# Optimization experiments

Measured on AMD Instinct MI355X. Metric: run time of the kernel, lower is better.

Reference implementation:

```python
import jax, jax.numpy as jnp
import numpy as np

N = 10000        # nodes
E = 320000       # edges (avg degree 32)
NF_IN = 256
NF_OUT = 512
EPS = 1e-5


def batch_norm(x, gamma, beta):
    # BatchNorm1d training-mode: biased stats over the node (batch) dim
    mu = jnp.mean(x, axis=0)
    var = jnp.var(x, axis=0)
    return (x - mu) * jax.lax.rsqrt(var + EPS) * gamma + beta


def sage_conv(x, src, dst, W_l, W_r, bias):
    # PyG SAGEConv, aggr='mean': out = lin_l(mean_{j->i} x_j) + lin_r(x_i)
    msg = x[src]                                             # [E, F]
    s = jax.ops.segment_sum(msg, dst, num_segments=N)        # [N, F]
    cnt = jax.ops.segment_sum(jnp.ones((msg.shape[0], 1), x.dtype), dst, num_segments=N)
    mean = s / jnp.maximum(cnt, 1.0)
    return mean @ W_l + bias + x @ W_r


def setup_inputs() -> dict:
    key = jax.random.key(0)
    ks = jax.random.split(key, 8)
    x = jax.random.normal(ks[0], (N, NF_IN), jnp.float32)
    edge_index = jax.random.randint(ks[1], (2, E), 0, N, dtype=jnp.int64)
    s_in = 0.02
    return {
        "x": x,
        "edge_index": edge_index,
        "gamma0": jnp.ones((NF_IN,), jnp.float32),
        "beta0": jnp.zeros((NF_IN,), jnp.float32),
        "W0_l": jax.random.normal(ks[2], (NF_IN, NF_OUT), jnp.float32) * s_in,
        "W0_r": jax.random.normal(ks[3], (NF_IN, NF_OUT), jnp.float32) * s_in,
        "bias0": jnp.zeros((NF_OUT,), jnp.float32),
        "gamma1": jnp.ones((NF_OUT,), jnp.float32),
        "beta1": jnp.zeros((NF_OUT,), jnp.float32),
        "W1_l": jax.random.normal(ks[4], (NF_OUT, NF_OUT), jnp.float32) * s_in,
        "W1_r": jax.random.normal(ks[5], (NF_OUT, NF_OUT), jnp.float32) * s_in,
        "bias1": jnp.zeros((NF_OUT,), jnp.float32),
        "W_sc": jax.random.normal(ks[6], (NF_IN, NF_OUT), jnp.float32) * s_in,
        "b_sc": jnp.zeros((NF_OUT,), jnp.float32),
    }


def reference(x, edge_index, gamma0, beta0, W0_l, W0_r, bias0,
              gamma1, beta1, W1_l, W1_r, bias1, W_sc, b_sc):
    src, dst = edge_index[0], edge_index[1]
    h = jax.nn.relu(batch_norm(x, gamma0, beta0))
    h = sage_conv(h, src, dst, W0_l, W0_r, bias0)
    h = jax.nn.relu(batch_norm(h, gamma1, beta1))
    h = sage_conv(h, src, dst, W1_l, W1_r, bias1)
    x_sc = x @ W_sc + b_sc  # nin_shortcut since nf_in != nf_out
    return x_sc + h
```

## Files before the change

kernel.cpp:

```cpp
#include <hip/hip_runtime.h>
#include <hip/hip_bf16.h>
#include <cstdint>
#include <cstddef>

#define N_NODES 10000
#define N_EDGES 320000
#define FIN 256
#define FOUT 512
#define BN_EPS 1e-5f
#define DEG_CAP 96
#define SLICE_CAP 18
#define NRANGES 20
#define NSLICES 16
#define NODES_PER_RANGE (N_NODES / NRANGES)
#define EDGES_PER_SLICE (N_EDGES / NSLICES)
#define SCAN_BLOCKS (NRANGES * NSLICES)

typedef unsigned short ushort_t;
typedef unsigned char uchar_t;
typedef __attribute__((ext_vector_type(8))) short short8;
typedef __attribute__((ext_vector_type(16))) float f32x16;
typedef __attribute__((ext_vector_type(2))) float f32x2;
typedef __attribute__((ext_vector_type(4))) unsigned short ushort4v;
typedef __attribute__((ext_vector_type(8))) unsigned short ushort8v;

__device__ inline ushort_t f2bf(float f) {
  __hip_bfloat16 h = __float2bfloat16(f);
  return *reinterpret_cast<ushort_t*>(&h);
}
__device__ inline float bf2f(ushort_t u) {
  union { unsigned int i; float f; } c;
  c.i = ((unsigned int)u) << 16;
  return c.f;
}
__device__ inline uchar_t f2q(float v) {
  return (uchar_t)(__builtin_amdgcn_cvt_pk_fp8_f32(v, v, 0u, false) & 0xffu);
}
__device__ inline void q4_to_f32(unsigned int w, float* o) {
  f32x2 lo = __builtin_amdgcn_cvt_pk_f32_fp8(w, false);
  f32x2 hi = __builtin_amdgcn_cvt_pk_f32_fp8(w, true);
  o[0] = lo[0]; o[1] = lo[1]; o[2] = hi[0]; o[3] = hi[1];
}

__global__ void zero_k(int* __restrict__ p, int n) {
  int i = blockIdx.x * blockDim.x + threadIdx.x;
  if (i < n) p[i] = 0;
}

__global__ __launch_bounds__(256)
void prologue_k(const int* __restrict__ src, const int* __restrict__ dst,
                int* __restrict__ fill, int* __restrict__ csrc,
                const float* __restrict__ W0l, const float* __restrict__ W0r,
                const float* __restrict__ Wsc, const float* __restrict__ W1l,
                const float* __restrict__ W1r, const float* __restrict__ bias1,
                const float* __restrict__ bsc,
                ushort_t* __restrict__ w0lt, ushort_t* __restrict__ w0rt,
                ushort_t* __restrict__ wsct, ushort_t* __restrict__ w1lt,
                ushort_t* __restrict__ w1rt, float* __restrict__ cbias,
                const float* __restrict__ x, float* __restrict__ sums0,
                ushort_t* __restrict__ xb, uchar_t* __restrict__ xq) {
  __shared__ __align__(16) char smem[512 * 4 + NODES_PER_RANGE * SLICE_CAP * 4];
  int b = blockIdx.x;
  int tid = threadIdx.x;

  if (b < SCAN_BLOCKS) {
    int range = b / NSLICES;
    int slice = b % NSLICES;
    int lo = range * NODES_PER_RANGE;
    int* lcnt = (int*)smem;
    int* lbuf = lcnt + 512;
    for (int i = tid; i < NODES_PER_RANGE; i += 256) lcnt[i] = 0;
    __syncthreads();

    int e0 = slice * EDGES_PER_SLICE;
    const int4* dst4 = (const int4*)(dst + e0);
    const int4* src4 = (const int4*)(src + e0);
    const int nvec = EDGES_PER_SLICE / 4;
    for (int v = tid; v < nvec; v += 256) {
      int4 d4 = dst4[v];
      int4 s4 = src4[v];
      int dd[4] = {d4.x, d4.y, d4.z, d4.w};
      int ss[4] = {s4.x, s4.y, s4.z, s4.w};
#pragma unroll
      for (int j = 0; j < 4; ++j) {
        int d = dd[j] - lo;
        if (d >= 0 && d < NODES_PER_RANGE) {
          int pos = atomicAdd(&lcnt[d], 1);
          if (pos < SLICE_CAP) lbuf[d * SLICE_CAP + pos] = ss[j];
        }
      }
    }
    __syncthreads();

    for (int i = tid; i < NODES_PER_RANGE; i += 256) {
      int cnt = min(lcnt[i], SLICE_CAP);
      if (cnt > 0) {
        int off = atomicAdd(&fill[lo + i], cnt);
        int wmax = min(cnt, DEG_CAP - off);
        for (int k = 0; k < wmax; ++k)
          csrc[(size_t)(lo + i) * DEG_CAP + off + k] = lbuf[i * SLICE_CAP + k];
      }
    }
    return;
  }

  if (b < SCAN_BLOCKS + 897) {
    int bb = b - SCAN_BLOCKS;
    if (bb == 896) {
      cbias[tid] = bias1[tid] + bsc[tid];
      cbias[tid + 256] = bias1[tid + 256] + bsc[tid + 256];
      return;
    }
    const float* W;
    ushort_t* Wt;
    int K, t;
    if (bb < 384) {
      K = 256; t = bb & 127;
      if (bb < 128)      { W = W0l; Wt = w0lt; }
      else if (bb < 256) { W = W0r; Wt = w0rt; }
      else               { W = Wsc; Wt = wsct; }
    } else {
      K = 512; t = (bb - 384) & 255;
      if (bb < 640) { W = W1l; Wt = w1lt; }
      else          { W = W1r; Wt = w1rt; }
    }
    ushort_t (*tl)[40] = (ushort_t(*)[40])smem;
    int Kt = K >> 5;
    int bk = (t % Kt) * 32, bn = (t / Kt) * 32;
    int tx = tid & 31, ty = tid >> 5;
#pragma unroll
    for (int i = 0; i < 4; ++i)
      tl[ty + i * 8][tx] = f2bf(W[(size_t)(bk + ty + i * 8) * 512 + bn + tx]);
    __syncthreads();
#pragma unroll
    for (int i = 0; i < 4; ++i)
      Wt[(size_t)(bn + ty + i * 8) * K + bk + tx] = tl[tx][ty + i * 8];
    return;
  }

  int blk = b - (SCAN_BLOCKS + 897);
  int c = tid;
  int r0 = blk * 80, r1 = r0 + 80;
  float s = 0.f, q = 0.f;
  for (int r = r0; r < r1; ++r) {
    float v = x[(size_t)r * FIN + c];
    s += v;
    q = fmaf(v, v, q);
    xb[(size_t)r * FIN + c] = f2bf(v);
    xq[(size_t)r * FIN + c] = f2q(v);
  }
  atomicAdd(&sums0[c], s);
  atomicAdd(&sums0[FIN + c], q);
}

template <int F>
__global__ __launch_bounds__(64)
void gather_mean_q8(const uchar_t* __restrict__ H, const int* __restrict__ fill,
                    const int* __restrict__ csrc, const float* __restrict__ sums,
                    const float* __restrict__ gamma, const float* __restrict__ beta,
                    float invN, ushort_t* __restrict__ agg) {
  constexpr int VEC = F / 64;
  int node = blockIdx.x;
  int c0 = threadIdx.x * VEC;
  float sc[VEC], sh[VEC];
#pragma unroll
  for (int j = 0; j < VEC; ++j) {
    float mu = sums[c0 + j] * invN;
    float var = fmaf(-mu, mu, sums[F + c0 + j] * invN);
    float s = rsqrtf(var + BN_EPS) * gamma[c0 + j];
    sc[j] = s;
    sh[j] = fmaf(-mu, s, beta[c0 + j]);
  }
  int deg = fill[node];
  int lim = min(deg, DEG_CAP);
  const int* cs = csrc + (size_t)node * DEG_CAP;
  float acc[VEC] = {};
  int e = 0;
  for (; e + 2 <= lim; e += 2) {
    int s0 = cs[e], s1 = cs[e + 1];
    float va[VEC], vb[VEC];
    if constexpr (VEC == 8) {
      uint2 ua = *(const uint2*)&H[(size_t)s0 * F + c0];
      uint2 ub = *(const uint2*)&H[(size_t)s1 * F + c0];
      q4_to_f32(ua.x, va); q4_to_f32(ua.y, va + 4);
      q4_to_f32(ub.x, vb); q4_to_f32(ub.y, vb + 4);
    } else {
      unsigned int ua = *(const unsigned int*)&H[(size_t)s0 * F + c0];
      unsigned int ub = *(const unsigned int*)&H[(size_t)s1 * F + c0];
      q4_to_f32(ua, va);
      q4_to_f32(ub, vb);
    }
#pragma unroll
    for (int j = 0; j < VEC; ++j)
      acc[j] += fmaxf(fmaf(va[j], sc[j], sh[j]), 0.f) +
                fmaxf(fmaf(vb[j], sc[j], sh[j]), 0.f);
  }
  if (e < lim) {
    int s0 = cs[e];
    float va[VEC];
    if constexpr (VEC == 8) {
      uint2 ua = *(const uint2*)&H[(size_t)s0 * F + c0];
      q4_to_f32(ua.x, va); q4_to_f32(ua.y, va + 4);
    } else {
      unsigned int ua = *(const unsigned int*)&H[(size_t)s0 * F + c0];
      q4_to_f32(ua, va);
    }
#pragma unroll
    for (int j = 0; j < VEC; ++j) acc[j] += fmaxf(fmaf(va[j], sc[j], sh[j]), 0.f);
  }
  float ic = 1.0f / fmaxf((float)deg, 1.0f);
  if constexpr (VEC == 8) {
    ushort8v o;
#pragma unroll
    for (int j = 0; j < 8; ++j) o[j] = f2bf(acc[j] * ic);
    *(ushort8v*)&agg[(size_t)node * F + c0] = o;
  } else {
    ushort4v o;
#pragma unroll
    for (int j = 0; j < 4; ++j) o[j] = f2bf(acc[j] * ic);
    *(ushort4v*)&agg[(size_t)node * F + c0] = o;
  }
}

template <int EPI, int K0, int K1, int K2, bool STATS, int BNS, int KBN, bool WQ>
__global__ __launch_bounds__(256)
void gemm_mfma(const ushort_t* __restrict__ A0, const ushort_t* __restrict__ B0,
               const ushort_t* __restrict__ A1p, const ushort_t* __restrict__ B1p,
               const ushort_t* __restrict__ A2p, const ushort_t* __restrict__ B2p,
               const float* __restrict__ bias, void* __restrict__ Cv,
               uchar_t* __restrict__ Cq, int M,
               const float* __restrict__ sums, const float* __restrict__ gamma,
               const float* __restrict__ beta, float invN,
               float* __restrict__ statsOut) {
  constexpr int ABYTES = 64 * 128;
  constexpr int BBYTES = 128 * 128;
  __shared__ __align__(16) char Asm[2 * ABYTES];
  __shared__ __align__(16) char Bsm[2 * BBYTES];
  __shared__ float ab_s[2 * KBN];

  int wgid = blockIdx.x;
  int cxcd = wgid & 7;
  int j = wgid >> 3;
  int nt = j & 3;
  int y = cxcd + (j >> 2) * 8;
  int MT = (M + 63) >> 6;
  if (y >= MT) return;
  int m0 = y * 64;
  int n0 = nt * 128;

  int tid = threadIdx.x;
  int lane = tid & 63;
  int w = tid >> 6;
  int wm = w >> 1, wn = w & 1;

  if constexpr (BNS >= 0) {
    for (int c = tid; c < KBN; c += 256) {
      float mu = sums[c] * invN;
      float var = fmaf(-mu, mu, sums[KBN + c] * invN);
      float s = rsqrtf(var + BN_EPS) * gamma[c];
      ab_s[c] = s;
      ab_s[KBN + c] = fmaf(-mu, s, beta[c]);
    }
    __syncthreads();
  }

  int ar = tid >> 2;
  int aqe = (tid & 3) * 16;
  int br = tid >> 1;
  int bqe = (tid & 1) * 32;
  bool arow_ok = (m0 + ar) < M;

  constexpr int NS = (K0 + K1 + K2) / 64;
  f32x16 acc0 = {}, acc1 = {};

  short8 ra[2], rb[4];
  bool dobn_cur = false;
  int aboff_cur = 0;

  auto LOADSTEP = [&](int ks) {
    int k0 = ks * 64;
    const ushort_t* Ap;
    const ushort_t* Bp;
    int lk, KA;
    if (k0 < K0) { Ap = A0; Bp = B0; lk = k0; KA = K0; dobn_cur = (BNS == 0); }
    else if (k0 < K0 + K1) { Ap = A1p; Bp = B1p; lk = k0 - K0; KA = K1; dobn_cur = (BNS == 1); }
    else { Ap = A2p; Bp = B2p; lk = k0 - K0 - K1; KA = K2; dobn_cur = (BNS == 2); }
    aboff_cur = lk;
    if (arow_ok) {
      const short8* ap = (const short8*)&Ap[(size_t)(m0 + ar) * KA + lk + aqe];
      ra[0] = ap[0]; ra[1] = ap[1];
    } else {
      ra[0] = short8{}; ra[1] = short8{};
    }
    const short8* bp = (const short8*)&Bp[(size_t)(n0 + br) * KA + lk + bqe];
    rb[0] = bp[0]; rb[1] = bp[1]; rb[2] = bp[2]; rb[3] = bp[3];
  };

  int aswz = (ar & 7) << 4;
  int bswz = (br & 7) << 4;

  auto STORESTEP = [&](int buf) {
    if constexpr (BNS >= 0) {
      if (dobn_cur && arow_ok) {
#pragma unroll
        for (int g = 0; g < 2; ++g) {
          const float* abp = &ab_s[aboff_cur + aqe + g * 8];
#pragma unroll
          for (int jj = 0; jj < 8; ++jj)
            ra[g][jj] = (short)f2bf(fmaxf(
                fmaf(bf2f((ushort_t)ra[g][jj]), abp[jj], abp[KBN + jj]), 0.f));
        }
      }
    }
    int abase = buf * ABYTES + ar * 128;
    int bbase = buf * BBYTES + br * 128;
#pragma unroll
    for (int g = 0; g < 2; ++g) {
      int cb = (aqe + g * 8) * 2;
      *(short8*)(Asm + abase + (cb ^ aswz)) = ra[g];
    }
#pragma unroll
    for (int g = 0; g < 4; ++g) {
      int cb = (bqe + g * 8) * 2;
      *(short8*)(Bsm + bbase + (cb ^ bswz)) = rb[g];
    }
  };

  LOADSTEP(0);
  STORESTEP(0);
  __syncthreads();

  int arow = wm * 32 + (lane & 31);
  int brow0 = wn * 64 + (lane & 31);
  int brow1 = brow0 + 32;
  int aswzr = (arow & 7) << 4;
  int bswzr = (brow0 & 7) << 4;

  for (int ks = 0; ks < NS; ++ks) {
    if (ks + 1 < NS) LOADSTEP(ks + 1);
    int abase = (ks & 1) * ABYTES + arow * 128;
    int bbase0 = (ks & 1) * BBYTES + brow0 * 128;
    int bbase1 = (ks & 1) * BBYTES + brow1 * 128;
#pragma unroll
    for (int kc = 0; kc < 4; ++kc) {
      int kb = kc * 32 + (lane >> 5) * 16;
      short8 af = *(const short8*)(Asm + abase + (kb ^ aswzr));
      short8 bf0 = *(const short8*)(Bsm + bbase0 + (kb ^ bswzr));
      short8 bf1 = *(const short8*)(Bsm + bbase1 + (kb ^ bswzr));
      acc0 = __builtin_amdgcn_mfma_f32_32x32x16_bf16(af, bf0, acc0, 0, 0, 0);
      acc1 = __builtin_amdgcn_mfma_f32_32x32x16_bf16(af, bf1, acc1, 0, 0, 0);
    }
    if (ks + 1 < NS) STORESTEP((ks + 1) & 1);
    __syncthreads();
  }

  float* st = (float*)Asm;
  if constexpr (STATS) {
    if (tid < 256) st[tid] = 0.f;
    __syncthreads();
  }

  int colb = n0 + wn * 64 + (lane & 31);
  int rquad = (lane >> 5) * 4;
#pragma unroll
  for (int ni = 0; ni < 2; ++ni) {
    int col = colb + ni * 32;
    float bv = bias[col];
    float s_l = 0.f, q_l = 0.f;
#pragma unroll
    for (int reg = 0; reg < 16; ++reg) {
      int row = m0 + wm * 32 + (reg & 3) + 8 * (reg >> 2) + rquad;
      if (row < M) {
        float v = (ni == 0 ? acc0[reg] : acc1[reg]) + bv;
        if constexpr (STATS) {
          s_l += v;
          q_l = fmaf(v, v, q_l);
        }
        if constexpr (EPI == 0) {
          ((ushort_t*)Cv)[(size_t)row * 512 + col] = f2bf(v);
          if constexpr (WQ) Cq[(size_t)row * 512 + col] = f2q(v);
        } else {
          ((float*)Cv)[(size_t)row * 512 + col] = v;
        }
      }
    }
    if constexpr (STATS) {
      int cloc = wn * 64 + ni * 32 + (lane & 31);
      atomicAdd(&st[cloc], s_l);
      atomicAdd(&st[128 + cloc], q_l);
    }
  }
  if constexpr (STATS) {
    __syncthreads();
    if (tid < 256) {
      int c = tid & 127;
      atomicAdd(&statsOut[(tid >> 7) * 512 + n0 + c], st[(tid >> 7) * 128 + c]);
    }
  }
}

extern "C" void kernel_launch(void* const* d_in, const int* in_sizes, int n_in,
                              void* d_out, int out_size, void* d_ws, size_t ws_size,
                              hipStream_t stream) {
  const float* x = (const float*)d_in[0];
  const int* ei = (const int*)d_in[1];
  const int* src = ei;
  const int* dst = ei + N_EDGES;
  const float* gamma0 = (const float*)d_in[2];
  const float* beta0  = (const float*)d_in[3];
  const float* W0l    = (const float*)d_in[4];
  const float* W0r    = (const float*)d_in[5];
  const float* bias0  = (const float*)d_in[6];
  const float* gamma1 = (const float*)d_in[7];
  const float* beta1  = (const float*)d_in[8];
  const float* W1l    = (const float*)d_in[9];
  const float* W1r    = (const float*)d_in[10];
  const float* bias1  = (const float*)d_in[11];
  const float* Wsc    = (const float*)d_in[12];
  const float* bsc    = (const float*)d_in[13];
  float* out = (float*)d_out;

  char* wp = (char*)d_ws;
  ushort_t* agg0b = (ushort_t*)wp; wp += (size_t)N_NODES * FIN * 2;
  ushort_t* h1b   = (ushort_t*)wp; wp += (size_t)N_NODES * FOUT * 2;
  ushort_t* agg1b = (ushort_t*)wp; wp += (size_t)N_NODES * FOUT * 2;
  ushort_t* xb    = (ushort_t*)wp; wp += (size_t)N_NODES * FIN * 2;
  uchar_t*  xq    = (uchar_t*)wp;  wp += (size_t)N_NODES * FIN;
  uchar_t*  h1q   = (uchar_t*)wp;  wp += (size_t)N_NODES * FOUT;
  ushort_t* w0lt  = (ushort_t*)wp; wp += (size_t)FIN * FOUT * 2;
  ushort_t* w0rt  = (ushort_t*)wp; wp += (size_t)FIN * FOUT * 2;
  ushort_t* wsct  = (ushort_t*)wp; wp += (size_t)FIN * FOUT * 2;
  ushort_t* w1lt  = (ushort_t*)wp; wp += (size_t)FOUT * FOUT * 2;
  ushort_t* w1rt  = (ushort_t*)wp; wp += (size_t)FOUT * FOUT * 2;
  float* cbias = (float*)wp; wp += FOUT * 4;
  float* sums0 = (float*)wp; wp += 2 * FIN * 4;
  float* sums1 = (float*)wp; wp += 2 * FOUT * 4;
  int* fill    = (int*)wp; wp += (size_t)N_NODES * 4;
  int* csrc    = (int*)wp; wp += (size_t)N_NODES * DEG_CAP * 4;

  const float invN = 1.0f / N_NODES;

  const int zwords = 2 * FIN + 2 * FOUT + N_NODES;
  zero_k<<<(zwords + 255) / 256, 256, 0, stream>>>((int*)sums0, zwords);

  prologue_k<<<SCAN_BLOCKS + 897 + 125, 256, 0, stream>>>(
      src, dst, fill, csrc, W0l, W0r, Wsc, W1l, W1r, bias1, bsc,
      w0lt, w0rt, wsct, w1lt, w1rt, cbias, x, sums0, xb, xq);

  gather_mean_q8<FIN><<<N_NODES, 64, 0, stream>>>(
      xq, fill, csrc, sums0, gamma0, beta0, invN, agg0b);

  const int GEMM_GRID = 8 * 4 * ((((N_NODES + 63) / 64) + 7) / 8);

  gemm_mfma<0, FIN, FIN, 0, true, 1, FIN, true>
      <<<GEMM_GRID, 256, 0, stream>>>(
      agg0b, w0lt, xb, w0rt, nullptr, nullptr, bias0, h1b, h1q, N_NODES,
      sums0, gamma0, beta0, invN, sums1);

  gather_mean_q8<FOUT><<<N_NODES, 64, 0, stream>>>(
      h1q, fill, csrc, sums1, gamma1, beta1, invN, agg1b);

  gemm_mfma<1, FOUT, FOUT, FIN, false, 1, FOUT, false>
      <<<GEMM_GRID, 256, 0, stream>>>(
      agg1b, w1lt, h1b, w1rt, xb, wsct, cbias, out, nullptr, N_NODES,
      sums1, gamma1, beta1, invN, nullptr);
}
```

Before: 121.9 us.

## Move own-feature BN into gather and stage GEMM tiles via direct global-to-LDS loads

The gather kernels now also apply BN+ReLU to each node's own features and write a normalized bf16 copy, so the GEMM no longer computes BN scales or transforms A tiles. GEMM tile staging is replaced by buffer global_load_lds writes straight into swizzled LDS, removing the register round trip and ds_write instructions. This adds extra global writes and reads of the normalized copies. It also drops the row bounds guard on A loads for the last partial tile.

```diff
diff --git a/kernel.cpp b/kernel.cpp
--- a/kernel.cpp
+++ b/kernel.cpp
@@ -40,6 +40,11 @@
   f32x2 lo = __builtin_amdgcn_cvt_pk_f32_fp8(w, false);
   f32x2 hi = __builtin_amdgcn_cvt_pk_f32_fp8(w, true);
   o[0] = lo[0]; o[1] = lo[1]; o[2] = hi[0]; o[3] = hi[1];
+}
+__device__ inline void gload_lds16(const void* g, void* l) {
+  __builtin_amdgcn_global_load_lds(
+      (const __attribute__((address_space(1))) unsigned int*)g,
+      (__attribute__((address_space(3))) unsigned int*)l, 16, 0, 0);
 }
 
 __global__ void zero_k(int* __restrict__ p, int n) {
@@ -153,12 +158,13 @@
   atomicAdd(&sums0[FIN + c], q);
 }
 
-template <int F>
+template <int F, bool OWNF32>
 __global__ __launch_bounds__(64)
 void gather_mean_q8(const uchar_t* __restrict__ H, const int* __restrict__ fill,
                     const int* __restrict__ csrc, const float* __restrict__ sums,
                     const float* __restrict__ gamma, const float* __restrict__ beta,
-                    float invN, ushort_t* __restrict__ agg) {
+                    float invN, ushort_t* __restrict__ agg,
+                    const void* __restrict__ ownsrc, ushort_t* __restrict__ ownout) {
   constexpr int VEC = F / 64;
   int node = blockIdx.x;
   int c0 = threadIdx.x * VEC;
@@ -171,6 +177,20 @@
     sc[j] = s;
     sh[j] = fmaf(-mu, s, beta[c0 + j]);
   }
+  if constexpr (OWNF32) {
+    const float* xr = (const float*)ownsrc + (size_t)node * F + c0;
+    ushort4v o;
+#pragma unroll
+    for (int j = 0; j < VEC; ++j) o[j] = f2bf(fmaxf(fmaf(xr[j], sc[j], sh[j]), 0.f));
+    *(ushort4v*)&ownout[(size_t)node * F + c0] = o;
+  } else {
+    ushort8v iv = *(const ushort8v*)((const ushort_t*)ownsrc + (size_t)node * F + c0);
+    ushort8v o;
+#pragma unroll
+    for (int j = 0; j < VEC; ++j) o[j] = f2bf(fmaxf(fmaf(bf2f(iv[j]), sc[j], sh[j]), 0.f));
+    *(ushort8v*)&ownout[(size_t)node * F + c0] = o;
+  }
+
   int deg = fill[node];
   int lim = min(deg, DEG_CAP);
   const int* cs = csrc + (size_t)node * DEG_CAP;
@@ -222,21 +242,17 @@
   }
 }
 
-template <int EPI, int K0, int K1, int K2, bool STATS, int BNS, int KBN, bool WQ>
+template <int EPI, int K0, int K1, int K2, bool STATS, bool WQ>
 __global__ __launch_bounds__(256)
-void gemm_mfma(const ushort_t* __restrict__ A0, const ushort_t* __restrict__ B0,
+void gemm_mfma(const ushort_t* __restrict__ A0p, const ushort_t* __restrict__ B0p,
                const ushort_t* __restrict__ A1p, const ushort_t* __restrict__ B1p,
                const ushort_t* __restrict__ A2p, const ushort_t* __restrict__ B2p,
                const float* __restrict__ bias, void* __restrict__ Cv,
-               uchar_t* __restrict__ Cq, int M,
-               const float* __restrict__ sums, const float* __restrict__ gamma,
-               const float* __restrict__ beta, float invN,
-               float* __restrict__ statsOut) {
+               uchar_t* __restrict__ Cq, int M, float* __restrict__ statsOut) {
   constexpr int ABYTES = 64 * 128;
   constexpr int BBYTES = 128 * 128;
   __shared__ __align__(16) char Asm[2 * ABYTES];
   __shared__ __align__(16) char Bsm[2 * BBYTES];
-  __shared__ float ab_s[2 * KBN];
 
   int wgid = blockIdx.x;
   int cxcd = wgid & 7;
@@ -253,82 +269,36 @@
   int w = tid >> 6;
   int wm = w >> 1, wn = w & 1;
 
-  if constexpr (BNS >= 0) {
-    for (int c = tid; c < KBN; c += 256) {
-      float mu = sums[c] * invN;
-      float var = fmaf(-mu, mu, sums[KBN + c] * invN);
-      float s = rsqrtf(var + BN_EPS) * gamma[c];
-      ab_s[c] = s;
-      ab_s[KBN + c] = fmaf(-mu, s, beta[c]);
-    }
-    __syncthreads();
-  }
-
-  int ar = tid >> 2;
-  int aqe = (tid & 3) * 16;
-  int br = tid >> 1;
-  int bqe = (tid & 1) * 32;
-  bool arow_ok = (m0 + ar) < M;
-
   constexpr int NS = (K0 + K1 + K2) / 64;
   f32x16 acc0 = {}, acc1 = {};
 
-  short8 ra[2], rb[4];
-  bool dobn_cur = false;
-  int aboff_cur = 0;
-
-  auto LOADSTEP = [&](int ks) {
-    int k0 = ks * 64;
+  int wbase = (tid & ~63) * 16;
+
+  auto STAGE = [&](int buf, int ks) {
+    int k0_ = ks * 64;
     const ushort_t* Ap;
     const ushort_t* Bp;
     int lk, KA;
-    if (k0 < K0) { Ap = A0; Bp = B0; lk = k0; KA = K0; dobn_cur = (BNS == 0); }
-    else if (k0 < K0 + K1) { Ap = A1p; Bp = B1p; lk = k0 - K0; KA = K1; dobn_cur = (BNS == 1); }
-    else { Ap = A2p; Bp = B2p; lk = k0 - K0 - K1; KA = K2; dobn_cur = (BNS == 2); }
-    aboff_cur = lk;
-    if (arow_ok) {
-      const short8* ap = (const short8*)&Ap[(size_t)(m0 + ar) * KA + lk + aqe];
-      ra[0] = ap[0]; ra[1] = ap[1];
-    } else {
-      ra[0] = short8{}; ra[1] = short8{};
-    }
-    const short8* bp = (const short8*)&Bp[(size_t)(n0 + br) * KA + lk + bqe];
-    rb[0] = bp[0]; rb[1] = bp[1]; rb[2] = bp[2]; rb[3] = bp[3];
+    if (k0_ < K0) { Ap = A0p; Bp = B0p; lk = k0_; KA = K0; }
+    else if (k0_ < K0 + K1) { Ap = A1p; Bp = B1p; lk = k0_ - K0; KA = K1; }
+    else { Ap = A2p; Bp = B2p; lk = k0_ - K0 - K1; KA = K2; }
+#pragma unroll
+    for (int i = 0; i < 2; ++i) {
+      int o = i * 4096 + tid * 16;
+      int row = o >> 7;
+      int chunk = (o >> 4) & 7;
+      const ushort_t* g = Ap + (size_t)(m0 + row) * KA + lk + ((chunk ^ (row & 7)) << 3);
+      gload_lds16(g, Asm + buf * ABYTES + i * 4096 + wbase);
+    }
+#pragma unroll
+    for (int i = 0; i < 4; ++i) {
+      int o = i * 4096 + tid * 16;
+      int row = o >> 7;
+      int chunk = (o >> 4) & 7;
+      const ushort_t* g = Bp + (size_t)(n0 + row) * KA + lk + ((chunk ^ (row & 7)) << 3);
+      gload_lds16(g, Bsm + buf * BBYTES + i * 4096 + wbase);
+    }
   };
-
-  int aswz = (ar & 7) << 4;
-  int bswz = (br & 7) << 4;
-
-  auto STORESTEP = [&](int buf) {
-    if constexpr (BNS >= 0) {
-      if (dobn_cur && arow_ok) {
-#pragma unroll
-        for (int g = 0; g < 2; ++g) {
-          const float* abp = &ab_s[aboff_cur + aqe + g * 8];
-#pragma unroll
-          for (int jj = 0; jj < 8; ++jj)
-            ra[g][jj] = (short)f2bf(fmaxf(
-                fmaf(bf2f((ushort_t)ra[g][jj]), abp[jj], abp[KBN + jj]), 0.f));
-        }
-      }
-    }
-    int abase = buf * ABYTES + ar * 128;
-    int bbase = buf * BBYTES + br * 128;
-#pragma unroll
-    for (int g = 0; g < 2; ++g) {
-      int cb = (aqe + g * 8) * 2;
-      *(short8*)(Asm + abase + (cb ^ aswz)) = ra[g];
-    }
-#pragma unroll
-    for (int g = 0; g < 4; ++g) {
-      int cb = (bqe + g * 8) * 2;
-      *(short8*)(Bsm + bbase + (cb ^ bswz)) = rb[g];
-    }
-  };
-
-  LOADSTEP(0);
-  STORESTEP(0);
-  __syncthreads();
 
   int arow = wm * 32 + (lane & 31);
   int brow0 = wn * 64 + (lane & 31);
@@ -336,8 +306,11 @@
   int aswzr = (arow & 7) << 4;
   int bswzr = (brow0 & 7) << 4;
 
+  STAGE(0, 0);
+  __syncthreads();
+
   for (int ks = 0; ks < NS; ++ks) {
-    if (ks + 1 < NS) LOADSTEP(ks + 1);
+    if (ks + 1 < NS) STAGE((ks + 1) & 1, ks + 1);
     int abase = (ks & 1) * ABYTES + arow * 128;
     int bbase0 = (ks & 1) * BBYTES + brow0 * 128;
     int bbase1 = (ks & 1) * BBYTES + brow1 * 128;
@@ -350,7 +323,6 @@
       acc0 = __builtin_amdgcn_mfma_f32_32x32x16_bf16(af, bf0, acc0, 0, 0, 0);
       acc1 = __builtin_amdgcn_mfma_f32_32x32x16_bf16(af, bf1, acc1, 0, 0, 0);
     }
-    if (ks + 1 < NS) STORESTEP((ks + 1) & 1);
     __syncthreads();
   }
 
@@ -422,7 +394,9 @@
 
   char* wp = (char*)d_ws;
   ushort_t* agg0b = (ushort_t*)wp; wp += (size_t)N_NODES * FIN * 2;
+  ushort_t* h0rb  = (ushort_t*)wp; wp += (size_t)N_NODES * FIN * 2;
   ushort_t* h1b   = (ushort_t*)wp; wp += (size_t)N_NODES * FOUT * 2;
+  ushort_t* h1rb  = (ushort_t*)wp; wp += (size_t)N_NODES * FOUT * 2;
   ushort_t* agg1b = (ushort_t*)wp; wp += (size_t)N_NODES * FOUT * 2;
   ushort_t* xb    = (ushort_t*)wp; wp += (size_t)N_NODES * FIN * 2;
   uchar_t*  xq    = (uchar_t*)wp;  wp += (size_t)N_NODES * FIN;
@@ -447,21 +421,19 @@
       src, dst, fill, csrc, W0l, W0r, Wsc, W1l, W1r, bias1, bsc,
       w0lt, w0rt, wsct, w1lt, w1rt, cbias, x, sums0, xb, xq);
 
-  gather_mean_q8<FIN><<<N_NODES, 64, 0, stream>>>(
-      xq, fill, csrc, sums0, gamma0, beta0, invN, agg0b);
+  gather_mean_q8<FIN, true><<<N_NODES, 64, 0, stream>>>(
+      xq, fill, csrc, sums0, gamma0, beta0, invN, agg0b, x, h0rb);
 
   const int GEMM_GRID = 8 * 4 * ((((N_NODES + 63) / 64) + 7) / 8);
 
-  gemm_mfma<0, FIN, FIN, 0, true, 1, FIN, true>
+  gemm_mfma<0, FIN, FIN, 0, true, true>
       <<<GEMM_GRID, 256, 0, stream>>>(
-      agg0b, w0lt, xb, w0rt, nullptr, nullptr, bias0, h1b, h1q, N_NODES,
-      sums0, gamma0, beta0, invN, sums1);
-
-  gather_mean_q8<FOUT><<<N_NODES, 64, 0, stream>>>(
-      h1q, fill, csrc, sums1, gamma1, beta1, invN, agg1b);
-
-  gemm_mfma<1, FOUT, FOUT, FIN, false, 1, FOUT, false>
+      agg0b, w0lt, h0rb, w0rt, nullptr, nullptr, bias0, h1b, h1q, N_NODES, sums1);
+
+  gather_mean_q8<FOUT, false><<<N_NODES, 64, 0, stream>>>(
+      h1q, fill, csrc, sums1, gamma1, beta1, invN, agg1b, h1b, h1rb);
+
+  gemm_mfma<1, FOUT, FOUT, FIN, false, false>
       <<<GEMM_GRID, 256, 0, stream>>>(
-      agg1b, w1lt, h1b, w1rt, xb, wsct, cbias, out, nullptr, N_NODES,
-      sums1, gamma1, beta1, invN, nullptr);
-}
+      agg1b, w1lt, h1rb, w1rt, xb, wsct, cbias, out, nullptr, N_NODES, nullptr);
+}
```

Result: faster. 115.4 us (-5.4%).
